# Optimization experiments

Hardware: AMD Instinct MI355X
Metric: run time of the kernel (lower is better)

Reference implementation:

```python
import jax, jax.numpy as jnp
import numpy as np

WALL, SRC_REAL, SRC_IMAG, DELAY_REAL, DELAY_IMAG = 0, 1, 2, 3, 4
DELAY_STEP = 8
MAX_PHASE_NORM = 2.0
READOUT_THRESHOLD = 0.35
PHASE_CLASSES = 8


def conv2d(x, w, b, pad):
    y = jax.lax.conv_general_dilated(x, w, (1, 1), [(pad, pad), (pad, pad)],
                                     dimension_numbers=('NCHW', 'OIHW', 'NCHW'))
    return y + b[None, :, None, None]


def clamp_phase(r, i):
    mag = jnp.sqrt(r * r + i * i + 1e-8)
    s = jnp.minimum(MAX_PHASE_NORM / mag, 1.0)
    return r * s, i * s


def neighbor_sum(x):
    # zero-padded 4-neighbor shift-and-sum stencil
    p = jnp.pad(x, ((0, 0), (0, 0), (1, 1), (1, 1)))
    return (p[:, :, 2:, 1:-1] + p[:, :, :-2, 1:-1] +
            p[:, :, 1:-1, 2:] + p[:, :, 1:-1, :-2])


def setup_inputs() -> dict:
    key = jax.random.key(0)
    ks = jax.random.split(key, 8)
    B, H, W, WD = 8, 256, 256, 32
    CIN = 6 + 4  # INPUT_CHANNELS + 4 (state_r, state_i, frontier_r, frontier_i)
    x = jax.random.normal(ks[0], (B, 6, H, W), jnp.float32)
    target = jax.random.randint(ks[1], (B, 2), 0, H)
    w_in = jax.random.normal(ks[2], (WD, CIN, 1, 1), jnp.float32) * (1.0 / np.sqrt(CIN))
    b_in = jnp.zeros((WD,), jnp.float32)
    w_up = jax.random.normal(ks[3], (WD, WD + CIN, 3, 3), jnp.float32) * (1.0 / np.sqrt((WD + CIN) * 9))
    b_up = jnp.zeros((WD,), jnp.float32)
    w_gate = jax.random.normal(ks[4], (1, WD + CIN, 1, 1), jnp.float32) * (1.0 / np.sqrt(WD + CIN))
    b_gate = jnp.zeros((1,), jnp.float32)
    angle = jnp.float32(0.0)
    decay_logit = jnp.float32(3.9)
    return dict(x=x, target=target, w_in=w_in, b_in=b_in, w_up=w_up, b_up=b_up,
                w_gate=w_gate, b_gate=b_gate, angle=angle, decay_logit=decay_logit, steps=16)


def reference(x, target, w_in, b_in, w_up, b_up, w_gate, b_gate, angle, decay_logit, steps):
    wall = x[:, WALL:WALL + 1]
    free = 1.0 - wall
    state_r = x[:, SRC_REAL:SRC_REAL + 1] * free
    state_i = x[:, SRC_IMAG:SRC_IMAG + 1] * free
    frontier_r, frontier_i = state_r, state_i
    h = jnp.tanh(conv2d(jnp.concatenate([x, state_r, state_i, frontier_r, frontier_i], 1), w_in, b_in, 0)) * free

    ang = jnp.tanh(angle) * 0.02
    cos_a, sin_a = jnp.cos(ang), jnp.sin(ang)
    decay = 0.95 + 0.05 * jax.nn.sigmoid(decay_logit)
    delay_r = x[:, DELAY_REAL:DELAY_REAL + 1]
    delay_i = x[:, DELAY_IMAG:DELAY_IMAG + 1]

    def body(carry, step):
        s_r, s_i, f_r, f_i, hh = carry
        inc_r = neighbor_sum(f_r)
        inc_i = neighbor_sum(f_i)
        is_delay = (step == DELAY_STEP).astype(x.dtype)
        inc_r = inc_r + is_delay * delay_r
        inc_i = inc_i + is_delay * delay_i
        source = jnp.concatenate([hh, x, s_r, s_i, f_r, f_i], 1)
        g = 0.998 + 0.002 * jax.nn.sigmoid(conv2d(source, w_gate, b_gate, 0))
        inc_r = inc_r * g
        inc_i = inc_i * g
        rot_r = inc_r * cos_a - inc_i * sin_a
        rot_i = inc_r * sin_a + inc_i * cos_a
        inc_r, inc_i = rot_r * free, rot_i * free
        inc_r, inc_i = clamp_phase(inc_r, inc_i)
        pre_wall = ((jnp.abs(inc_r) + jnp.abs(inc_i)) * wall).mean()
        s_r, s_i = clamp_phase(decay * s_r + inc_r, decay * s_i + inc_i)
        s_r = s_r * free
        s_i = s_i * free
        hh = jnp.tanh(0.8 * hh + conv2d(source, w_up, b_up, 1)) * free
        st = jnp.concatenate([s_r, s_i], 1)
        return (s_r, s_i, inc_r, inc_i, hh), (st, pre_wall)

    carry0 = (state_r, state_i, frontier_r, frontier_i, h)
    _, (sts, pre_walls) = jax.lax.scan(body, carry0, jnp.arange(1, steps + 1))
    state0 = jnp.concatenate([state_r, state_i], 1)
    states = jnp.concatenate([state0[None], sts], 0)  # [steps+1, B, 2, H, W]
    final = states[-1]

    diffs = states[1:] - states[:-1]
    delta = jnp.mean(jnp.sqrt(jnp.mean(diffs ** 2, axis=(1, 2, 3, 4))))
    norm_by_step = jnp.mean(jnp.sqrt(jnp.sum(states ** 2, axis=2)))
    sat = (jnp.abs(final) > 4.0).astype(jnp.float32).mean()
    pw = pre_walls.mean()
    norm = jnp.sqrt(jnp.sum(final ** 2, axis=1, keepdims=True))
    leak = ((norm > 0.5) & (wall > 0.5)).astype(jnp.float32).mean()
    stats = jnp.stack([delta, norm_by_step, sat, pw, leak])

    b = jnp.arange(final.shape[0])
    vec = final[b, :, target[:, 0], target[:, 1]]  # [B, 2]
    k = jnp.arange(PHASE_CLASSES)
    theta = 2.0 * jnp.pi * k / PHASE_CLASSES
    phases = jnp.stack([jnp.cos(theta), jnp.sin(theta)], axis=1)  # [K, 2]
    mag = jnp.sqrt(jnp.sum(vec ** 2, axis=1) + 1e-8)
    none = (READOUT_THRESHOLD - mag) * 12.0
    phase_logits = (vec @ phases.T - READOUT_THRESHOLD) * 12.0
    logits = jnp.concatenate([none[:, None], phase_logits], axis=1)
    return logits, stats
```

## Files before the change

kernel.cpp:

```cpp
#include <hip/hip_runtime.h>
#include <hip/hip_bf16.h>

#define HW2D 65536
#define NPIX 524288
#define NB 8
#define PW 258
#define PP 66564
#define NSTEPS 16
#define RHH 2064
#define RTT 4128
#define ROWB 8256

typedef __hip_bfloat16 bf16;
typedef unsigned long long u64;
typedef __attribute__((ext_vector_type(8))) short short8;
typedef __attribute__((ext_vector_type(4))) float f32x4;

__device__ __forceinline__ unsigned short f2bfu(float v){
  bf16 h = __float2bfloat16(v); return *(unsigned short*)&h;
}
__device__ __forceinline__ float tanh_a(float z){
  return z*__builtin_amdgcn_rsqf(fmaf(z, z, 1.0f));
}
__device__ __forceinline__ float fast_sigmoid(float z){
  return 1.0f/(1.0f + __expf(-z));
}
__device__ __forceinline__ unsigned char f2fp8(float v){
  return (unsigned char)(__builtin_amdgcn_cvt_pk_fp8_f32(v, 0.f, 0, false) & 0xFF);
}
__device__ __forceinline__ int chmap(int m){ return (m>>1) + (m&1)*16; }

__global__ void k_prep(const float* angle, const float* decay_logit,
                       float* ST, float* PRM){
  int t = threadIdx.x;
  for (int i = t; i < 64*32; i += 256) ST[i] = 0.0f;
  if (t == 0){
    float ang = tanhf(angle[0])*0.02f;
    PRM[0] = cosf(ang);
    PRM[1] = sinf(ang);
    PRM[2] = 0.95f + 0.05f/(1.0f+expf(-decay_logit[0]));
  }
}

__global__ void k_wprep(const float* __restrict__ w_up, const float* __restrict__ w_gate,
                        u64* __restrict__ WB8, short8* __restrict__ WB16){
  int t = threadIdx.x;
  int lane = t & 63;
  int r_ = lane & 15, g = lane >> 4;
  for (int slot = t>>6; slot < 19; slot += 4){
    u64 v = 0;
    #pragma unroll
    for (int j=0;j<8;j++){
      float w = 0.f;
      int ch = chmap(g*8+j);
      if (slot < 18){
        int tile = slot/9, s = slot%9;
        int oc = tile*16 + r_;
        int dy=s/3, dx=s%3;
        w = w_up[((oc*42+ch)*3+dy)*3+dx];
        if (s==4 && oc==ch) w += 0.8f;
      } else {
        if (r_==0) w = w_gate[ch];
      }
      v |= ((u64)f2fp8(w)) << (8*j);
    }
    WB8[slot*64+lane] = v;
  }
  for (int slot = t>>6; slot < 11; slot += 4){
    short8 v;
    #pragma unroll
    for (int j=0;j<8;j++){
      float w = 0.f;
      int tt = (g&1)*8 + j;
      int tapsel = g>>1;
      if (slot < 10){
        int tile = slot/5, s2 = slot%5;
        int tap = 2*s2 + tapsel;
        int oc = tile*16 + r_;
        if (tap <= 8 && tt < 10){
          int src = (tt<4) ? (38+tt) : (32+(tt-4));
          int dy=tap/3, dx=tap%3;
          w = w_up[((oc*42+src)*3+dy)*3+dx];
        }
      } else {
        if (r_==0 && tapsel==0 && tt<10){
          int src = (tt<4) ? (38+tt) : (32+(tt-4));
          w = w_gate[src];
        }
      }
      v[j] = (short)f2bfu(w);
    }
    WB16[slot*64+lane] = v;
  }
}

__global__ void k_border(unsigned char* HH0, unsigned char* HH1,
                         unsigned char* TAIL0, unsigned char* TAIL1){
  int i = blockIdx.x*256 + threadIdx.x;
  if (i >= NB*PP) return;
  int b = i / PP, pp_ = i % PP;
  int row = pp_ / PW, col = pp_ % PW;
  if (row != 0 && row != 257 && col != 0 && col != 257) return;
  size_t rb = (size_t)(b*PW + row);
  #pragma unroll
  for (int g=0; g<4; g++){
    size_t a = (rb*4+g)*RHH + (size_t)col*8;
    *(uint2*)(HH0+a) = (uint2){0,0};
    *(uint2*)(HH1+a) = (uint2){0,0};
  }
  #pragma unroll
  for (int h=0; h<2; h++){
    size_t a = (rb*2+h)*RTT + (size_t)col*16;
    *(uint4*)(TAIL0+a) = (uint4){0,0,0,0};
    *(uint4*)(TAIL1+a) = (uint4){0,0,0,0};
  }
}

__global__ void k_init(const float* __restrict__ x, const float* __restrict__ w_in,
                       const float* __restrict__ b_in,
                       float2* __restrict__ S0, float2* __restrict__ F0,
                       float* __restrict__ WALL,
                       unsigned char* __restrict__ HH0, unsigned char* __restrict__ TAIL0,
                       unsigned char* __restrict__ TAIL1, float* ST){
  int tid = threadIdx.x;
  int p = blockIdx.x*256 + tid;
  int b = p >> 16, rem = p & 65535;
  int y = rem >> 8, xc = rem & 255;
  const float* xb = x + (size_t)b*6*HW2D;
  float wall = xb[rem];
  float fre = 1.0f - wall;
  float s_r = xb[HW2D + rem]*fre;
  float s_i = xb[2*HW2D + rem]*fre;
  S0[p] = (float2){s_r, s_i};
  F0[p] = (float2){s_r, s_i};
  WALL[p] = wall;
  float src10[10];
  src10[0]=wall;
  #pragma unroll
  for (int c=1;c<6;c++) src10[c]=xb[c*HW2D+rem];
  src10[6]=s_r; src10[7]=s_i; src10[8]=s_r; src10[9]=s_i;
  float hv[32];
  #pragma unroll
  for (int c=0;c<32;c++){
    float a = b_in[c];
    #pragma unroll
    for (int k=0;k<10;k++) a += w_in[c*10+k]*src10[k];
    hv[c] = tanh_a(a)*fre;
  }
  unsigned int words[8];
  #pragma unroll
  for (int w=0;w<8;w++){
    int lo = __builtin_amdgcn_cvt_pk_fp8_f32(hv[2*w], hv[16+2*w], 0, false);
    words[w] = (unsigned int)__builtin_amdgcn_cvt_pk_fp8_f32(hv[2*w+1], hv[17+2*w], lo, true);
  }
  size_t rb = (size_t)(b*PW + y + 1);
  #pragma unroll
  for (int g=0; g<4; g++){
    *(uint2*)(HH0 + (rb*4+g)*RHH + (size_t)(xc+1)*8) = (uint2){words[2*g], words[2*g+1]};
  }
  unsigned short tv[16];
  tv[0]=f2bfu(s_r); tv[1]=f2bfu(s_i); tv[2]=f2bfu(s_r); tv[3]=f2bfu(s_i);
  #pragma unroll
  for (int c=0;c<6;c++) tv[4+c] = f2bfu(src10[c]);
  #pragma unroll
  for (int c=10;c<16;c++) tv[c] = 0;
  #pragma unroll
  for (int h=0; h<2; h++){
    short8 v;
    #pragma unroll
    for (int j=0;j<8;j++) v[j] = (short)tv[h*8+j];
    *(short8*)(TAIL0 + (rb*2+h)*RTT + (size_t)(xc+1)*16) = v;
    *(short8*)(TAIL1 + (rb*2+h)*RTT + (size_t)(xc+1)*16) = v;
  }
  float v = __builtin_amdgcn_sqrtf(s_r*s_r + s_i*s_i);
  #pragma unroll
  for (int off=32; off>0; off>>=1) v += __shfl_down(v, off);
  __shared__ float red[4];
  int wid = tid >> 6;
  if ((tid&63)==0) red[wid] = v;
  __syncthreads();
  if (tid==0) atomicAdd(&ST[(blockIdx.x & 63)*32 + 16], red[0]+red[1]+red[2]+red[3]);
}

__global__ __launch_bounds__(256) void k_step(
    const unsigned char* __restrict__ HHo, unsigned char* __restrict__ HHn,
    const unsigned char* __restrict__ TAILo, unsigned char* __restrict__ TAILn,
    const float2* __restrict__ So, float2* __restrict__ Sn,
    const float2* __restrict__ Fo, float2* __restrict__ Fn,
    const float* __restrict__ WALL,
    const u64* __restrict__ WB8, const short8* __restrict__ WB16,
    const float* __restrict__ b_up, const float* __restrict__ x,
    const float* __restrict__ b_gate, const float* __restrict__ PRM,
    float* ST, int step){
  __shared__ float lgate[256];
  __shared__ float red[3][4];
  int bid = blockIdx.x;
  int b = bid & 7, y = bid >> 3;
  int tid = threadIdx.x;
  int wv = tid >> 6, lane = tid & 63;
  int r_ = lane & 15, g = lane >> 4;
  int px0 = wv*64 + r_;

  int p = b*HW2D + (y<<8) + tid;
  float2 sc = So[p];
  float2 fup = (y>0)    ? Fo[p-256] : (float2){0.f,0.f};
  float2 fdn = (y<255)  ? Fo[p+256] : (float2){0.f,0.f};
  float2 flt = (tid>0)  ? Fo[p-1]   : (float2){0.f,0.f};
  float2 frt = (tid<255)? Fo[p+1]   : (float2){0.f,0.f};
  float dlr = 0.f, dli = 0.f;
  if (step==8){
    const float* xb = x + (size_t)b*6*HW2D;
    int rem = (y<<8)+tid;
    dlr = xb[3*HW2D+rem]; dli = xb[4*HW2D+rem];
  }
  float wallB = WALL[p];
  float ca = PRM[0], sa = PRM[1], dec = PRM[2];

  const unsigned char* Hrow = HHo + (size_t)(b*PW + y)*ROWB + (size_t)g*RHH + (size_t)px0*8;
  const unsigned char* Trow = TAILo + (size_t)(b*PW + y)*ROWB + (size_t)(g&1)*RTT + (size_t)px0*16;
  const unsigned char* Tzero = TAILo + (size_t)(b*PW)*ROWB + (size_t)(g&1)*RTT + (size_t)px0*16;
  int gb = g >> 1;
  const unsigned char* tb0 = Trow + (size_t)((0+gb)/3)*ROWB + (size_t)((0+gb)%3)*16;
  const unsigned char* tb1 = Trow + (size_t)((2+gb)/3)*ROWB + (size_t)((2+gb)%3)*16;
  const unsigned char* tb2 = Trow + (size_t)((4+gb)/3)*ROWB + (size_t)((4+gb)%3)*16;
  const unsigned char* tb3 = Trow + (size_t)((6+gb)/3)*ROWB + (size_t)((6+gb)%3)*16;
  const unsigned char* tb4 = gb ? Tzero : (Trow + 2*ROWB + 2*16);
  const u64* wb8l = WB8 + lane;
  const short8* wb16l = WB16 + lane;

  f32x4 acc[4][2], accg[4];
  #pragma unroll
  for (int mt=0;mt<4;mt++){
    acc[mt][0] = (f32x4){0.f,0.f,0.f,0.f};
    acc[mt][1] = (f32x4){0.f,0.f,0.f,0.f};
    accg[mt]   = (f32x4){0.f,0.f,0.f,0.f};
  }

  #pragma unroll
  for (int s=0;s<9;s++){
    u64 b0 = wb8l[s*64], b1 = wb8l[(9+s)*64];
    u64 aH[4];
    #pragma unroll
    for (int mt=0;mt<4;mt++)
      aH[mt] = *(const u64*)(Hrow + (size_t)((s/3)*ROWB) + ((s%3)*8 + mt*128));
    #pragma unroll
    for (int mt=0;mt<4;mt++){
      acc[mt][0] = __builtin_amdgcn_mfma_f32_16x16x32_fp8_fp8((long)b0, (long)aH[mt], acc[mt][0], 0,0,0);
      acc[mt][1] = __builtin_amdgcn_mfma_f32_16x16x32_fp8_fp8((long)b1, (long)aH[mt], acc[mt][1], 0,0,0);
    }
    if (s==4){
      u64 bg = wb8l[18*64];
      #pragma unroll
      for (int mt=0;mt<4;mt++)
        accg[mt] = __builtin_amdgcn_mfma_f32_16x16x32_fp8_fp8((long)bg, (long)aH[mt], accg[mt], 0,0,0);
    }
  }
  #pragma unroll
  for (int s2=0;s2<5;s2++){
    short8 b0 = wb16l[s2*64], b1 = wb16l[(5+s2)*64];
    const unsigned char* tb = (s2==0)?tb0:(s2==1)?tb1:(s2==2)?tb2:(s2==3)?tb3:tb4;
    short8 aT[4];
    #pragma unroll
    for (int mt=0;mt<4;mt++)
      aT[mt] = *(const short8*)(tb + mt*256);
    #pragma unroll
    for (int mt=0;mt<4;mt++){
      acc[mt][0] = __builtin_amdgcn_mfma_f32_16x16x32_bf16(b0, aT[mt], acc[mt][0], 0,0,0);
      acc[mt][1] = __builtin_amdgcn_mfma_f32_16x16x32_bf16(b1, aT[mt], acc[mt][1], 0,0,0);
    }
    if (s2==2){
      short8 bgt = wb16l[10*64];
      #pragma unroll
      for (int mt=0;mt<4;mt++)
        accg[mt] = __builtin_amdgcn_mfma_f32_16x16x32_bf16(bgt, aT[mt], accg[mt], 0,0,0);
    }
  }
  if (lane < 16){
    #pragma unroll
    for (int mt=0;mt<4;mt++) lgate[wv*64 + mt*16 + lane] = accg[mt][0];
  }

  const float* wallrow = WALL + (size_t)b*HW2D + (y<<8);
  const float4* bup4 = (const float4*)b_up;
  float4 bb0 = bup4[g];
  float4 bb1 = bup4[4+g];
  unsigned char* Hn = HHn + ((size_t)(b*PW + y + 1)*4 + g)*RHH;
  #pragma unroll
  for (int mt=0;mt<4;mt++){
    int px = px0 + mt*16;
    float fre = 1.0f - wallrow[px];
    float tA0 = tanh_a(acc[mt][0][0] + bb0.x)*fre;
    float tB0 = tanh_a(acc[mt][1][0] + bb1.x)*fre;
    float tA1 = tanh_a(acc[mt][0][1] + bb0.y)*fre;
    float tB1 = tanh_a(acc[mt][1][1] + bb1.y)*fre;
    float tA2 = tanh_a(acc[mt][0][2] + bb0.z)*fre;
    float tB2 = tanh_a(acc[mt][1][2] + bb1.z)*fre;
    float tA3 = tanh_a(acc[mt][0][3] + bb0.w)*fre;
    float tB3 = tanh_a(acc[mt][1][3] + bb1.w)*fre;
    int w0 = __builtin_amdgcn_cvt_pk_fp8_f32(tA0, tB0, 0, false);
    w0 = __builtin_amdgcn_cvt_pk_fp8_f32(tA1, tB1, w0, true);
    int w1 = __builtin_amdgcn_cvt_pk_fp8_f32(tA2, tB2, 0, false);
    w1 = __builtin_amdgcn_cvt_pk_fp8_f32(tA3, tB3, w1, true);
    *(uint2*)(Hn + (size_t)(px+1)*8) = (uint2){(unsigned)w0, (unsigned)w1};
  }

  __builtin_amdgcn_sched_barrier(0);
  asm volatile("s_waitcnt lgkmcnt(0)" ::: "memory");
  __builtin_amdgcn_s_barrier();
  __builtin_amdgcn_sched_barrier(0);

  float s_r = sc.x, s_i = sc.y;
  float incr = fup.x + fdn.x + flt.x + frt.x + dlr;
  float inci = fup.y + fdn.y + flt.y + frt.y + dli;
  float fre = 1.0f - wallB;
  float a = lgate[tid] + b_gate[0];
  float gg = 0.998f + 0.002f*fast_sigmoid(a);
  incr *= gg; inci *= gg;
  float rr = incr*ca - inci*sa;
  float ri = incr*sa + inci*ca;
  incr = rr*fre; inci = ri*fre;
  float m1 = fmaf(incr,incr, fmaf(inci,inci, 1e-8f));
  float sc2 = fminf(2.0f*__builtin_amdgcn_rsqf(m1), 1.0f);
  incr *= sc2; inci *= sc2;
  float pw = (fabsf(incr)+fabsf(inci))*wallB;
  float nr = dec*s_r + incr, ni = dec*s_i + inci;
  float m2 = fmaf(nr,nr, fmaf(ni,ni, 1e-8f));
  sc2 = fminf(2.0f*__builtin_amdgcn_rsqf(m2), 1.0f);
  nr = nr*sc2*fre; ni = ni*sc2*fre;
  Sn[p] = (float2){nr, ni};
  Fn[p] = (float2){incr, inci};
  ushort4 pk;
  pk.x = f2bfu(nr); pk.y = f2bfu(ni); pk.z = f2bfu(incr); pk.w = f2bfu(inci);
  *(ushort4*)(TAILn + (size_t)(b*PW + y + 1)*ROWB + (size_t)(tid+1)*16) = pk;
  float d2 = (nr-s_r)*(nr-s_r)+(ni-s_i)*(ni-s_i);
  float nrm = __builtin_amdgcn_sqrtf(nr*nr+ni*ni);
  #pragma unroll
  for (int off=32; off>0; off>>=1){
    d2  += __shfl_down(d2, off);
    nrm += __shfl_down(nrm, off);
    pw  += __shfl_down(pw, off);
  }
  int wid = tid >> 6;
  if ((tid&63)==0){ red[0][wid]=d2; red[1][wid]=nrm; red[2][wid]=pw; }
  __syncthreads();
  if (tid==0){
    float* st = ST + (bid & 63)*32;
    atomicAdd(&st[step-1], red[0][0]+red[0][1]+red[0][2]+red[0][3]);
    atomicAdd(&st[16],     red[1][0]+red[1][1]+red[1][2]+red[1][3]);
    atomicAdd(&st[17],     red[2][0]+red[2][1]+red[2][2]+red[2][3]);
  }
}

__global__ void k_tail(const float* __restrict__ WALL, const float2* __restrict__ S,
                       float* ST){
  int tid = threadIdx.x;
  int p = blockIdx.x*256 + tid;
  float wall = WALL[p];
  float2 c = S[p];
  float vr = c.x, vi = c.y;
  float sat = (fabsf(vr)>4.0f ? 1.0f:0.0f) + (fabsf(vi)>4.0f ? 1.0f:0.0f);
  float nrm = __builtin_amdgcn_sqrtf(vr*vr+vi*vi);
  float leak = (nrm>0.5f && wall>0.5f) ? 1.0f : 0.0f;
  #pragma unroll
  for (int off=32; off>0; off>>=1){
    sat  += __shfl_down(sat, off);
    leak += __shfl_down(leak, off);
  }
  __shared__ float red[2][4];
  int wid = tid >> 6;
  if ((tid&63)==0){ red[0][wid]=sat; red[1][wid]=leak; }
  __syncthreads();
  if (tid==0){
    float* st = ST + (blockIdx.x & 63)*32;
    atomicAdd(&st[18], red[0][0]+red[0][1]+red[0][2]+red[0][3]);
    atomicAdd(&st[19], red[1][0]+red[1][1]+red[1][2]+red[1][3]);
  }
}

__global__ void k_final(const float2* __restrict__ S, const int* __restrict__ target,
                        const float* __restrict__ ST, float* __restrict__ out){
  int t = threadIdx.x;
  if (t < 8){
    int ty = target[2*t], tx = target[2*t+1];
    int p = (t<<16) + (ty<<8) + tx;
    float2 c = S[p];
    float vr = c.x, vi = c.y;
    float mag = sqrtf(vr*vr+vi*vi+1e-8f);
    out[t*9] = (0.35f - mag)*12.0f;
    #pragma unroll
    for (int k=0;k<8;k++){
      float th = 6.283185307179586f * (float)k / 8.0f;
      out[t*9+1+k] = (vr*cosf(th)+vi*sinf(th) - 0.35f)*12.0f;
    }
  }
  float tot[20];
  #pragma unroll
  for (int i=0;i<20;i++){
    float v = ST[t*32 + i];
    #pragma unroll
    for (int off=32; off>0; off>>=1) v += __shfl_down(v, off);
    tot[i] = v;
  }
  if (t == 0){
    float d = 0.0f;
    #pragma unroll
    for (int s=0;s<16;s++) d += sqrtf(tot[s]/1048576.0f);
    out[72] = d/16.0f;
    out[73] = tot[16]/8912896.0f;
    out[74] = tot[18]/1048576.0f;
    out[75] = tot[17]/(524288.0f*16.0f);
    out[76] = tot[19]/524288.0f;
  }
}

extern "C" void kernel_launch(void* const* d_in, const int* in_sizes, int n_in,
                              void* d_out, int out_size, void* d_ws, size_t ws_size,
                              hipStream_t stream) {
  const float* x       = (const float*)d_in[0];
  const int*   target  = (const int*)  d_in[1];
  const float* w_in    = (const float*)d_in[2];
  const float* b_in    = (const float*)d_in[3];
  const float* w_up    = (const float*)d_in[4];
  const float* b_up    = (const float*)d_in[5];
  const float* w_gate  = (const float*)d_in[6];
  const float* b_gate  = (const float*)d_in[7];
  const float* angle   = (const float*)d_in[8];
  const float* decay_l = (const float*)d_in[9];
  float* out = (float*)d_out;

  char* ws = (char*)d_ws;
  size_t off = 0;
  unsigned char* HH0 = (unsigned char*)(ws+off); off += (size_t)NB*PP*32;
  unsigned char* HH1 = (unsigned char*)(ws+off); off += (size_t)NB*PP*32;
  unsigned char* TAIL0=(unsigned char*)(ws+off); off += (size_t)NB*PP*32;
  unsigned char* TAIL1=(unsigned char*)(ws+off); off += (size_t)NB*PP*32;
  float2* S0 = (float2*)(ws+off); off += (size_t)NPIX*8;
  float2* S1 = (float2*)(ws+off); off += (size_t)NPIX*8;
  float2* F0 = (float2*)(ws+off); off += (size_t)NPIX*8;
  float2* F1 = (float2*)(ws+off); off += (size_t)NPIX*8;
  float* WALL = (float*)(ws+off); off += (size_t)NPIX*4;
  u64* WB8 = (u64*)(ws+off); off += (size_t)19*64*8;
  short8* WB16 = (short8*)(ws+off); off += (size_t)11*64*16;
  float* ST = (float*)(ws+off); off += (size_t)64*32*4;
  float* PRM = (float*)(ws+off); off += 16*4;

  k_prep<<<1,256,0,stream>>>(angle, decay_l, ST, PRM);
  k_wprep<<<1,256,0,stream>>>(w_up, w_gate, WB8, WB16);
  k_border<<<(NB*PP+255)/256,256,0,stream>>>(HH0, HH1, TAIL0, TAIL1);
  k_init<<<NPIX/256,256,0,stream>>>(x, w_in, b_in, S0, F0, WALL, HH0, TAIL0, TAIL1, ST);

  unsigned char *hho=HH0, *hhn=HH1, *tlo=TAIL0, *tln=TAIL1;
  float2 *so=S0, *sn=S1, *fo=F0, *fn=F1;
  for (int t=1;t<=NSTEPS;t++){
    k_step<<<2048,256,0,stream>>>(hho, hhn, tlo, tln, so, sn, fo, fn, WALL,
                                  WB8, WB16, b_up, x, b_gate, PRM, ST, t);
    unsigned char* tc=hho; hho=hhn; hhn=tc;
    tc=tlo; tlo=tln; tln=tc;
    float2* tf=so; so=sn; sn=tf;
    tf=fo; fo=fn; fn=tf;
  }
  k_tail<<<NPIX/256,256,0,stream>>>(WALL, so, ST);
  k_final<<<1,64,0,stream>>>(so, target, ST, out);
}
```

Baseline: 549.8 us.

## Drop fp32 state/frontier buffers, read bf16 copies from tail tensor

Removes the separate fp32 state and frontier arrays and instead reads the bf16-packed state and frontier already stored in the padded TAIL buffer. The goal is to cut global traffic (16 bytes written and about 40 bytes read per pixel per step) and the extra stores. It also replaces the LDS gate exchange and block barrier with a wave shuffle, and turns block-level reductions into per-wave atomics. The trade-off is that the recurrence now carries bf16-rounded state, so errors can accumulate across steps, and there are more atomics.

Result: no change. 542.3 us (-1.4%).

```diff
diff --git a/kernel.cpp b/kernel.cpp
--- a/kernel.cpp
+++ b/kernel.cpp
@@ -19,6 +19,8 @@
 __device__ __forceinline__ unsigned short f2bfu(float v){
   bf16 h = __float2bfloat16(v); return *(unsigned short*)&h;
 }
+__device__ __forceinline__ float blo(unsigned int w){ return __uint_as_float(w<<16); }
+__device__ __forceinline__ float bhi(unsigned int w){ return __uint_as_float(w & 0xffff0000u); }
 __device__ __forceinline__ float tanh_a(float z){
   return z*__builtin_amdgcn_rsqf(fmaf(z, z, 1.0f));
 }
@@ -118,7 +120,6 @@
 
 __global__ void k_init(const float* __restrict__ x, const float* __restrict__ w_in,
                        const float* __restrict__ b_in,
-                       float2* __restrict__ S0, float2* __restrict__ F0,
                        float* __restrict__ WALL,
                        unsigned char* __restrict__ HH0, unsigned char* __restrict__ TAIL0,
                        unsigned char* __restrict__ TAIL1, float* ST){
@@ -131,8 +132,6 @@
   float fre = 1.0f - wall;
   float s_r = xb[HW2D + rem]*fre;
   float s_i = xb[2*HW2D + rem]*fre;
-  S0[p] = (float2){s_r, s_i};
-  F0[p] = (float2){s_r, s_i};
   WALL[p] = wall;
   float src10[10];
   src10[0]=wall;
@@ -175,25 +174,17 @@
   float v = __builtin_amdgcn_sqrtf(s_r*s_r + s_i*s_i);
   #pragma unroll
   for (int off=32; off>0; off>>=1) v += __shfl_down(v, off);
-  __shared__ float red[4];
-  int wid = tid >> 6;
-  if ((tid&63)==0) red[wid] = v;
-  __syncthreads();
-  if (tid==0) atomicAdd(&ST[(blockIdx.x & 63)*32 + 16], red[0]+red[1]+red[2]+red[3]);
+  if ((tid&63)==0) atomicAdd(&ST[(blockIdx.x & 63)*32 + 16], v);
 }
 
 __global__ __launch_bounds__(256) void k_step(
     const unsigned char* __restrict__ HHo, unsigned char* __restrict__ HHn,
     const unsigned char* __restrict__ TAILo, unsigned char* __restrict__ TAILn,
-    const float2* __restrict__ So, float2* __restrict__ Sn,
-    const float2* __restrict__ Fo, float2* __restrict__ Fn,
     const float* __restrict__ WALL,
     const u64* __restrict__ WB8, const short8* __restrict__ WB16,
     const float* __restrict__ b_up, const float* __restrict__ x,
     const float* __restrict__ b_gate, const float* __restrict__ PRM,
     float* ST, int step){
-  __shared__ float lgate[256];
-  __shared__ float red[3][4];
   int bid = blockIdx.x;
   int b = bid & 7, y = bid >> 3;
   int tid = threadIdx.x;
@@ -201,19 +192,19 @@
   int r_ = lane & 15, g = lane >> 4;
   int px0 = wv*64 + r_;
 
-  int p = b*HW2D + (y<<8) + tid;
-  float2 sc = So[p];
-  float2 fup = (y>0)    ? Fo[p-256] : (float2){0.f,0.f};
-  float2 fdn = (y<255)  ? Fo[p+256] : (float2){0.f,0.f};
-  float2 flt = (tid>0)  ? Fo[p-1]   : (float2){0.f,0.f};
-  float2 frt = (tid<255)? Fo[p+1]   : (float2){0.f,0.f};
+  const unsigned char* Tc = TAILo + (size_t)(b*PW + y + 1)*ROWB + (size_t)(tid+1)*16;
+  unsigned int sw  = *(const unsigned int*)(Tc);
+  unsigned int fu  = *(const unsigned int*)(Tc - ROWB + 4);
+  unsigned int fd  = *(const unsigned int*)(Tc + ROWB + 4);
+  unsigned int fl  = *(const unsigned int*)(Tc - 16 + 4);
+  unsigned int fr2 = *(const unsigned int*)(Tc + 16 + 4);
   float dlr = 0.f, dli = 0.f;
   if (step==8){
     const float* xb = x + (size_t)b*6*HW2D;
     int rem = (y<<8)+tid;
     dlr = xb[3*HW2D+rem]; dli = xb[4*HW2D+rem];
   }
-  float wallB = WALL[p];
+  float wallB = WALL[b*HW2D + (y<<8) + tid];
   float ca = PRM[0], sa = PRM[1], dec = PRM[2];
 
   const unsigned char* Hrow = HHo + (size_t)(b*PW + y)*ROWB + (size_t)g*RHH + (size_t)px0*8;
@@ -275,10 +266,12 @@
         accg[mt] = __builtin_amdgcn_mfma_f32_16x16x32_bf16(bgt, aT[mt], accg[mt], 0,0,0);
     }
   }
-  if (lane < 16){
-    #pragma unroll
-    for (int mt=0;mt<4;mt++) lgate[wv*64 + mt*16 + lane] = accg[mt][0];
-  }
+
+  float ga0 = __shfl(accg[0][0], r_);
+  float ga1 = __shfl(accg[1][0], r_);
+  float ga2 = __shfl(accg[2][0], r_);
+  float ga3 = __shfl(accg[3][0], r_);
+  float gpre = (g==0) ? ga0 : (g==1) ? ga1 : (g==2) ? ga2 : ga3;
 
   const float* wallrow = WALL + (size_t)b*HW2D + (y<<8);
   const float4* bup4 = (const float4*)b_up;
@@ -304,16 +297,11 @@
     *(uint2*)(Hn + (size_t)(px+1)*8) = (uint2){(unsigned)w0, (unsigned)w1};
   }
 
-  __builtin_amdgcn_sched_barrier(0);
-  asm volatile("s_waitcnt lgkmcnt(0)" ::: "memory");
-  __builtin_amdgcn_s_barrier();
-  __builtin_amdgcn_sched_barrier(0);
-
-  float s_r = sc.x, s_i = sc.y;
-  float incr = fup.x + fdn.x + flt.x + frt.x + dlr;
-  float inci = fup.y + fdn.y + flt.y + frt.y + dli;
+  float s_r = blo(sw), s_i = bhi(sw);
+  float incr = blo(fu) + blo(fd) + blo(fl) + blo(fr2) + dlr;
+  float inci = bhi(fu) + bhi(fd) + bhi(fl) + bhi(fr2) + dli;
   float fre = 1.0f - wallB;
-  float a = lgate[tid] + b_gate[0];
+  float a = gpre + b_gate[0];
   float gg = 0.998f + 0.002f*fast_sigmoid(a);
   incr *= gg; inci *= gg;
   float rr = incr*ca - inci*sa;
@@ -327,8 +315,6 @@
   float m2 = fmaf(nr,nr, fmaf(ni,ni, 1e-8f));
   sc2 = fminf(2.0f*__builtin_amdgcn_rsqf(m2), 1.0f);
   nr = nr*sc2*fre; ni = ni*sc2*fre;
-  Sn[p] = (float2){nr, ni};
-  Fn[p] = (float2){incr, inci};
   ushort4 pk;
   pk.x = f2bfu(nr); pk.y = f2bfu(ni); pk.z = f2bfu(incr); pk.w = f2bfu(inci);
   *(ushort4*)(TAILn + (size_t)(b*PW + y + 1)*ROWB + (size_t)(tid+1)*16) = pk;
@@ -340,24 +326,23 @@
     nrm += __shfl_down(nrm, off);
     pw  += __shfl_down(pw, off);
   }
-  int wid = tid >> 6;
-  if ((tid&63)==0){ red[0][wid]=d2; red[1][wid]=nrm; red[2][wid]=pw; }
-  __syncthreads();
-  if (tid==0){
-    float* st = ST + (bid & 63)*32;
-    atomicAdd(&st[step-1], red[0][0]+red[0][1]+red[0][2]+red[0][3]);
-    atomicAdd(&st[16],     red[1][0]+red[1][1]+red[1][2]+red[1][3]);
-    atomicAdd(&st[17],     red[2][0]+red[2][1]+red[2][2]+red[2][3]);
-  }
-}
-
-__global__ void k_tail(const float* __restrict__ WALL, const float2* __restrict__ S,
+  if (lane==0){
+    float* st = ST + ((bid*4+wv) & 63)*32;
+    atomicAdd(&st[step-1], d2);
+    atomicAdd(&st[16],     nrm);
+    atomicAdd(&st[17],     pw);
+  }
+}
+
+__global__ void k_tail(const float* __restrict__ WALL, const unsigned char* __restrict__ TAIL,
                        float* ST){
   int tid = threadIdx.x;
   int p = blockIdx.x*256 + tid;
+  int b = p >> 16, rem = p & 65535;
+  int row = (rem>>8)+1, col = (rem&255)+1;
+  unsigned int sw = *(const unsigned int*)(TAIL + (size_t)(b*PW+row)*ROWB + (size_t)col*16);
+  float vr = blo(sw), vi = bhi(sw);
   float wall = WALL[p];
-  float2 c = S[p];
-  float vr = c.x, vi = c.y;
   float sat = (fabsf(vr)>4.0f ? 1.0f:0.0f) + (fabsf(vi)>4.0f ? 1.0f:0.0f);
   float nrm = __builtin_amdgcn_sqrtf(vr*vr+vi*vi);
   float leak = (nrm>0.5f && wall>0.5f) ? 1.0f : 0.0f;
@@ -366,25 +351,20 @@
     sat  += __shfl_down(sat, off);
     leak += __shfl_down(leak, off);
   }
-  __shared__ float red[2][4];
-  int wid = tid >> 6;
-  if ((tid&63)==0){ red[0][wid]=sat; red[1][wid]=leak; }
-  __syncthreads();
-  if (tid==0){
-    float* st = ST + (blockIdx.x & 63)*32;
-    atomicAdd(&st[18], red[0][0]+red[0][1]+red[0][2]+red[0][3]);
-    atomicAdd(&st[19], red[1][0]+red[1][1]+red[1][2]+red[1][3]);
-  }
-}
-
-__global__ void k_final(const float2* __restrict__ S, const int* __restrict__ target,
+  if ((tid&63)==0){
+    float* st = ST + ((blockIdx.x*4+(tid>>6)) & 63)*32;
+    atomicAdd(&st[18], sat);
+    atomicAdd(&st[19], leak);
+  }
+}
+
+__global__ void k_final(const unsigned char* __restrict__ TAIL, const int* __restrict__ target,
                         const float* __restrict__ ST, float* __restrict__ out){
   int t = threadIdx.x;
   if (t < 8){
     int ty = target[2*t], tx = target[2*t+1];
-    int p = (t<<16) + (ty<<8) + tx;
-    float2 c = S[p];
-    float vr = c.x, vi = c.y;
+    unsigned int sw = *(const unsigned int*)(TAIL + (size_t)(t*PW+ty+1)*ROWB + (size_t)(tx+1)*16);
+    float vr = blo(sw), vi = bhi(sw);
     float mag = sqrtf(vr*vr+vi*vi+1e-8f);
     out[t*9] = (0.35f - mag)*12.0f;
     #pragma unroll
@@ -434,10 +414,6 @@
   unsigned char* HH1 = (unsigned char*)(ws+off); off += (size_t)NB*PP*32;
   unsigned char* TAIL0=(unsigned char*)(ws+off); off += (size_t)NB*PP*32;
   unsigned char* TAIL1=(unsigned char*)(ws+off); off += (size_t)NB*PP*32;
-  float2* S0 = (float2*)(ws+off); off += (size_t)NPIX*8;
-  float2* S1 = (float2*)(ws+off); off += (size_t)NPIX*8;
-  float2* F0 = (float2*)(ws+off); off += (size_t)NPIX*8;
-  float2* F1 = (float2*)(ws+off); off += (size_t)NPIX*8;
   float* WALL = (float*)(ws+off); off += (size_t)NPIX*4;
   u64* WB8 = (u64*)(ws+off); off += (size_t)19*64*8;
   short8* WB16 = (short8*)(ws+off); off += (size_t)11*64*16;
@@ -447,18 +423,15 @@
   k_prep<<<1,256,0,stream>>>(angle, decay_l, ST, PRM);
   k_wprep<<<1,256,0,stream>>>(w_up, w_gate, WB8, WB16);
   k_border<<<(NB*PP+255)/256,256,0,stream>>>(HH0, HH1, TAIL0, TAIL1);
-  k_init<<<NPIX/256,256,0,stream>>>(x, w_in, b_in, S0, F0, WALL, HH0, TAIL0, TAIL1, ST);
+  k_init<<<NPIX/256,256,0,stream>>>(x, w_in, b_in, WALL, HH0, TAIL0, TAIL1, ST);
 
   unsigned char *hho=HH0, *hhn=HH1, *tlo=TAIL0, *tln=TAIL1;
-  float2 *so=S0, *sn=S1, *fo=F0, *fn=F1;
   for (int t=1;t<=NSTEPS;t++){
-    k_step<<<2048,256,0,stream>>>(hho, hhn, tlo, tln, so, sn, fo, fn, WALL,
+    k_step<<<2048,256,0,stream>>>(hho, hhn, tlo, tln, WALL,
                                   WB8, WB16, b_up, x, b_gate, PRM, ST, t);
     unsigned char* tc=hho; hho=hhn; hhn=tc;
     tc=tlo; tlo=tln; tln=tc;
-    float2* tf=so; so=sn; sn=tf;
-    tf=fo; fo=fn; fn=tf;
-  }
-  k_tail<<<NPIX/256,256,0,stream>>>(WALL, so, ST);
-  k_final<<<1,64,0,stream>>>(so, target, ST, out);
-}
+  }
+  k_tail<<<NPIX/256,256,0,stream>>>(WALL, tlo, ST);
+  k_final<<<1,64,0,stream>>>(tlo, target, ST, out);
+}
```
